# Optimization experiments

Measured on AMD Instinct MI355X. Metric: run time of the kernel, lower is better.

Reference implementation:

```python
import jax, jax.numpy as jnp
import numpy as np

B, N, M = 4, 1024, 3072          # batch, latent (query) len, prefix context len
D, H, DH, L, F = 512, 8, 64, 6, 2048  # dim, heads, dim_head, depth, ff hidden
SCALE = DH ** -0.5


def _ln(x, g, b):
    m = jnp.mean(x, axis=-1, keepdims=True)
    v = jnp.mean(jnp.square(x - m), axis=-1, keepdims=True)
    return (x - m) * jax.lax.rsqrt(v + 1e-5) * g + b


def _heads(t):  # [b, n, h*d] -> [b, h, n, d]
    b, n, _ = t.shape
    return t.reshape(b, n, H, DH).transpose(0, 2, 1, 3)


def _attend(q, k, v):
    # q:[b,h,i,d], k/v:[b,h,j,d]; causal mask triu(j-i+1) as in source
    i, j = q.shape[2], k.shape[2]
    sim = jnp.einsum('bhid,bhjd->bhij', q * SCALE, k)
    mask = jnp.triu(jnp.ones((i, j), dtype=bool), j - i + 1)
    sim = jnp.where(mask, -jnp.finfo(sim.dtype).max, sim)
    attn = jax.nn.softmax(sim, axis=-1)
    out = jnp.einsum('bhij,bhjd->bhid', attn, v)
    return out.transpose(0, 2, 1, 3).reshape(q.shape[0], i, H * DH)


def _ff(x, g, b, w1, w2):
    return jax.nn.gelu(_ln(x, g, b) @ w1, approximate=False) @ w2


def setup_inputs() -> dict:
    key = jax.random.key(0)
    ks = jax.random.split(key, 12)
    rn = lambda k, shape: jax.random.normal(k, shape, dtype=jnp.float32) * 0.02
    return {
        'x': jax.random.normal(ks[0], (B, N, D), jnp.float32),
        'context': jax.random.normal(ks[1], (B, M, D), jnp.float32),
        'pa_norm_g': jnp.ones((D,), jnp.float32), 'pa_norm_b': jnp.zeros((D,), jnp.float32),
        'pa_cnorm_g': jnp.ones((D,), jnp.float32), 'pa_cnorm_b': jnp.zeros((D,), jnp.float32),
        'pa_wq': rn(ks[2], (D, H * DH)), 'pa_wkv': rn(ks[3], (D, 2 * H * DH)),
        'pa_wo': rn(ks[4], (H * DH, D)), 'pa_wo_b': jnp.zeros((D,), jnp.float32),
        'pf_ln_g': jnp.ones((D,), jnp.float32), 'pf_ln_b': jnp.zeros((D,), jnp.float32),
        'pf_w1': rn(ks[5], (D, F)), 'pf_w2': rn(ks[6], (F, D)),
        'sa_ln_g': jnp.ones((L, D), jnp.float32), 'sa_ln_b': jnp.zeros((L, D), jnp.float32),
        'sa_wqkv': rn(ks[7], (L, D, 3 * H * DH)), 'sa_wo': rn(ks[8], (L, H * DH, D)),
        'sf_ln_g': jnp.ones((L, D), jnp.float32), 'sf_ln_b': jnp.zeros((L, D), jnp.float32),
        'sf_w1': rn(ks[9], (L, D, F)), 'sf_w2': rn(ks[10], (L, F, D)),
    }


def reference(x, context, pa_norm_g, pa_norm_b, pa_cnorm_g, pa_cnorm_b,
              pa_wq, pa_wkv, pa_wo, pa_wo_b, pf_ln_g, pf_ln_b, pf_w1, pf_w2,
              sa_ln_g, sa_ln_b, sa_wqkv, sa_wo, sf_ln_g, sf_ln_b, sf_w1, sf_w2):
    # --- CausalPrefixAttention (eval mode: no dropout, context_mask=None) ---
    xn = _ln(x, pa_norm_g, pa_norm_b)
    cn = _ln(context, pa_cnorm_g, pa_cnorm_b)
    q = _heads(xn @ pa_wq)
    k_in, v_in = jnp.split(xn @ pa_wkv, 2, axis=-1)
    k_c, v_c = jnp.split(cn @ pa_wkv, 2, axis=-1)
    k = _heads(jnp.concatenate([k_c, k_in], axis=1))  # [b,h,M+N,d]
    v = _heads(jnp.concatenate([v_c, v_in], axis=1))
    x = _attend(q, k, v) @ pa_wo + pa_wo_b + x
    x = _ff(x, pf_ln_g, pf_ln_b, pf_w1, pf_w2) + x
    # --- depth x (CausalAttention + FeedForward) ---
    for l in range(L):
        xn = _ln(x, sa_ln_g[l], sa_ln_b[l])
        qq, kk, vv = jnp.split(xn @ sa_wqkv[l], 3, axis=-1)
        x = _attend(_heads(qq), _heads(kk), _heads(vv)) @ sa_wo[l] + x
        x = _ff(x, sf_ln_g[l], sf_ln_b[l], sf_w1[l], sf_w2[l]) + x
    return x
```

## Files before the change

### kernel.cpp

```cpp
#include <hip/hip_runtime.h>
#include <hip/hip_bf16.h>
#include <cstdint>
#include <cstddef>

typedef __bf16 bf16;
typedef __attribute__((ext_vector_type(8))) __bf16 bf16x8;
typedef __attribute__((ext_vector_type(4))) __bf16 bf16x4;
typedef __attribute__((ext_vector_type(4))) float f32x4;

constexpr int B_ = 4, QN = 1024, MCTX = 3072, D_ = 512, H_ = 8, DHE = 64, L_ = 6, FF_ = 2048;
constexpr float SCL2_ = 0.18033688011f;

__device__ __forceinline__ f32x4 mfma16(bf16x8 a, bf16x8 b, f32x4 c) {
  return __builtin_amdgcn_mfma_f32_16x16x32_bf16(a, b, c, 0, 0, 0);
}

__device__ __forceinline__ void gl_lds16(const bf16* g, bf16* l) {
  __builtin_amdgcn_global_load_lds((const __attribute__((address_space(1))) void*)g,
                                   (__attribute__((address_space(3))) void*)l, 16, 0, 0);
}

__device__ __forceinline__ float fexp2(float x) {
  float r;
  asm("v_exp_f32 %0, %1" : "=v"(r) : "v"(x));
  return r;
}

__global__ __launch_bounds__(256) void ln_kernel(const float* __restrict__ x,
                                                 const float* __restrict__ g,
                                                 const float* __restrict__ b,
                                                 bf16* __restrict__ out, int rows) {
  int wid = threadIdx.x >> 6, lane = threadIdx.x & 63;
  int row = blockIdx.x * 4 + wid;
  if (row >= rows) return;
  const float* xr = x + (size_t)row * D_;
  f32x4 a0 = *(const f32x4*)(xr + lane * 8);
  f32x4 a1 = *(const f32x4*)(xr + lane * 8 + 4);
  float s = 0.f;
#pragma unroll
  for (int i = 0; i < 4; i++) { s += a0[i]; s += a1[i]; }
#pragma unroll
  for (int d = 1; d < 64; d <<= 1) s += __shfl_xor(s, d);
  float mean = s * (1.0f / 512.0f);
  float q = 0.f;
#pragma unroll
  for (int i = 0; i < 4; i++) {
    float t0 = a0[i] - mean, t1 = a1[i] - mean;
    q += t0 * t0 + t1 * t1;
  }
#pragma unroll
  for (int d = 1; d < 64; d <<= 1) q += __shfl_xor(q, d);
  float rstd = rsqrtf(q * (1.0f / 512.0f) + 1e-5f);
  f32x4 g0 = *(const f32x4*)(g + lane * 8);
  f32x4 g1 = *(const f32x4*)(g + lane * 8 + 4);
  f32x4 b0 = *(const f32x4*)(b + lane * 8);
  f32x4 b1 = *(const f32x4*)(b + lane * 8 + 4);
  bf16x8 o;
#pragma unroll
  for (int i = 0; i < 4; i++) {
    o[i] = (bf16)((a0[i] - mean) * rstd * g0[i] + b0[i]);
    o[i + 4] = (bf16)((a1[i] - mean) * rstd * g1[i] + b1[i]);
  }
  *(bf16x8*)(out + (size_t)row * D_ + lane * 8) = o;
}

struct WDesc { const float* src; bf16* dst; int K; int N; int tstart; };
struct WPack { WDesc d[30]; int n; };

__global__ __launch_bounds__(256) void wtrans_all(WPack p) {
  __shared__ float tile[64][65];
  const int bid = blockIdx.x;
  int mi = 0;
  for (int i = 1; i < p.n; i++)
    if (p.d[i].tstart <= bid) mi = i;
  const float* src = p.d[mi].src;
  bf16* dst = p.d[mi].dst;
  const int K = p.d[mi].K, N = p.d[mi].N;
  const int lt = bid - p.d[mi].tstart;
  const int ntx = N >> 6;
  const int n0 = (lt % ntx) * 64, k0 = (lt / ntx) * 64;
  const int tx = threadIdx.x, ty = threadIdx.y;
#pragma unroll
  for (int pp = 0; pp < 16; pp++)
    tile[pp * 4 + ty][tx] = src[(size_t)(k0 + pp * 4 + ty) * N + n0 + tx];
  __syncthreads();
#pragma unroll
  for (int pp = 0; pp < 16; pp++)
    dst[(size_t)(n0 + pp * 4 + ty) * K + k0 + tx] = (bf16)tile[tx][pp * 4 + ty];
}

template <int EPI>
__global__ __launch_bounds__(256) void gemm128(const bf16* __restrict__ A,
                                               const bf16* __restrict__ BT,
                                               void* __restrict__ C0,
                                               void* __restrict__ C1,
                                               void* __restrict__ C2,
                                               const float* __restrict__ resid,
                                               const float* __restrict__ bias,
                                               int M, int N, int K, int vstr) {
  __shared__ bf16 smA[2][128 * 64];
  __shared__ bf16 smB[2][128 * 64];
  const int tid = threadIdx.x, wid = tid >> 6, lane = tid & 63;
  const int lr = lane & 15, lg = lane >> 4;
  const int tm = blockIdx.y * 128, tn = blockIdx.x * 128;
  const int wr = (wid >> 1) * 64, wc = (wid & 1) * 64;

  const int l3 = lane >> 3;
  const int kslot = ((lane & 7) ^ l3) * 8;
  const bf16* gA[4];
  const bf16* gB[4];
#pragma unroll
  for (int j = 0; j < 4; j++) {
    gA[j] = A + (size_t)(tm + wid * 32 + j * 8 + l3) * K + kslot;
    gB[j] = BT + (size_t)(tn + wid * 32 + j * 8 + l3) * K + kslot;
  }

  f32x4 acc[4][4] = {};
  const int nt = K >> 6;

  auto stage = [&](int bi, int kt) {
#pragma unroll
    for (int j = 0; j < 4; j++) {
      gl_lds16(gA[j] + kt, &smA[bi][(wid * 32 + j * 8) * 64]);
      gl_lds16(gB[j] + kt, &smB[bi][(wid * 32 + j * 8) * 64]);
    }
  };

  stage(0, 0);
  int buf = 0;
  for (int t = 0; t < nt; ++t) {
    asm volatile("s_waitcnt vmcnt(0)" ::: "memory");
    __builtin_amdgcn_s_barrier();
    __builtin_amdgcn_sched_barrier(0);
    if (t + 1 < nt) stage(buf ^ 1, (t + 1) * 64);

    bf16x8 af[4][2], bfr[4][2];
#pragma unroll
    for (int i = 0; i < 4; i++) {
      const int row = wr + i * 16 + lr;
#pragma unroll
      for (int kk = 0; kk < 2; kk++)
        af[i][kk] = *(const bf16x8*)(&smA[buf][row * 64 + (((kk * 4 + lg) ^ (row & 7)) * 8)]);
    }
#pragma unroll
    for (int j = 0; j < 4; j++) {
      const int row = wc + j * 16 + lr;
#pragma unroll
      for (int kk = 0; kk < 2; kk++)
        bfr[j][kk] = *(const bf16x8*)(&smB[buf][row * 64 + (((kk * 4 + lg) ^ (row & 7)) * 8)]);
    }
#pragma unroll
    for (int kk = 0; kk < 2; kk++)
#pragma unroll
      for (int i = 0; i < 4; i++)
#pragma unroll
        for (int j = 0; j < 4; j++)
          acc[i][j] = mfma16(af[i][kk], bfr[j][kk], acc[i][j]);
    buf ^= 1;
  }

  const bool row_major_dst =
      (EPI == 1) || (EPI == 3 && tn < 1024) || (EPI == 4 && tn < 1024) || (EPI == 5 && tn < 512);
  if (row_major_dst) {
    bf16* dst;
    int dstr, rbase, coff;
    if (EPI == 1) { dst = (bf16*)C0; dstr = N; rbase = tm; coff = tn; }
    else if (EPI == 3) {
      if (tn < 512) { dst = (bf16*)C0; dstr = 512; rbase = tm; coff = tn; }
      else { dst = (bf16*)C1; dstr = 1024; rbase = (tm >> 10) * 4096 + (tm & 1023) + 3072; coff = tn - 512; }
    } else if (EPI == 4) { dst = (bf16*)C0; dstr = 1536; rbase = tm; coff = tn; }
    else { dst = (bf16*)C1; dstr = 1024; rbase = (tm / 3072) * 4096 + (tm % 3072); coff = tn; }

    __syncthreads();
    bf16* lb = &smA[0][0];
#pragma unroll
    for (int i = 0; i < 4; i++) {
#pragma unroll
      for (int r = 0; r < 4; r++) {
        const int row = wr + i * 16 + lg * 4 + r;
#pragma unroll
        for (int j = 0; j < 4; j++) {
          const int col = wc + j * 16 + lr;
          float v = acc[i][j][r];
          if (EPI == 1) {
            float u = v * (0.7978845608f + 0.0356774081f * v * v);
            float e = fexp2(fminf(2.885390082f * u, 80.0f));
            v = v * e / (1.0f + e);
          }
          lb[row * 128 + (col ^ ((row & 7) << 3))] = (bf16)v;
        }
      }
    }
    __syncthreads();
#pragma unroll
    for (int p = 0; p < 8; p++) {
      const int row = p * 16 + (tid >> 4);
      const int cb = (tid & 15) * 8;
      bf16x8 v = *(const bf16x8*)&lb[row * 128 + (cb ^ ((row & 7) << 3))];
      *(bf16x8*)&dst[(size_t)(rbase + row) * dstr + coff + cb] = v;
    }
  } else {
#pragma unroll
    for (int i = 0; i < 4; i++) {
      const int row = tm + wr + i * 16 + lg * 4;
#pragma unroll
      for (int j = 0; j < 4; j++) {
        const int col = tn + wc + j * 16 + lr;
        bf16x4 pk = {(bf16)acc[i][j][0], (bf16)acc[i][j][1],
                     (bf16)acc[i][j][2], (bf16)acc[i][j][3]};
        if (EPI == 3) {
          const int cc = col - 1024, hh = cc >> 6, dh = cc & 63;
          const int bb = row >> 10, s = (row & 1023) + 3072;
          *(bf16x4*)&((bf16*)C2)[((size_t)(bb * 8 + hh) * 64 + dh) * vstr + s] = pk;
        } else if (EPI == 4) {
          const int cc = col - 1024, hh = cc >> 6, dh = cc & 63;
          const int bb = row >> 10, s = row & 1023;
          *(bf16x4*)&((bf16*)C2)[((size_t)(bb * 8 + hh) * 64 + dh) * vstr + s] = pk;
        } else {
          const int bq = row / 3072, s = row - bq * 3072;
          const int cc = col - 512, hh = cc >> 6, dh = cc & 63;
          *(bf16x4*)&((bf16*)C2)[((size_t)(bq * 8 + hh) * 64 + dh) * vstr + s] = pk;
        }
      }
    }
  }
}

__global__ __launch_bounds__(256) void gemm64_res(const bf16* __restrict__ A,
                                                  const bf16* __restrict__ BT,
                                                  float* __restrict__ Cout,
                                                  const float* __restrict__ resid,
                                                  const float* __restrict__ bias,
                                                  int M, int N, int K) {
  __shared__ bf16 smA[3][64 * 64];
  __shared__ bf16 smB[3][64 * 64];
  const int tid = threadIdx.x, wid = tid >> 6, lane = tid & 63;
  const int lr = lane & 15, lg = lane >> 4;
  const int tm = blockIdx.y * 64, tn = blockIdx.x * 64;
  const int wr = (wid >> 1) * 32, wc = (wid & 1) * 32;

  const int l3 = lane >> 3;
  const int kslot = ((lane & 7) ^ l3) * 8;
  const int row0 = 2 * wid * 8 + l3;
  const bf16* gA0 = A + (size_t)(tm + row0) * K + kslot;
  const bf16* gA1 = A + (size_t)(tm + row0 + 8) * K + kslot;
  const bf16* gB0 = BT + (size_t)(tn + row0) * K + kslot;
  const bf16* gB1 = BT + (size_t)(tn + row0 + 8) * K + kslot;

  f32x4 acc[2][2] = {};
  const int nt = K >> 6;

  auto stage = [&](int bi, int kt) {
    gl_lds16(gA0 + kt, &smA[bi][(2 * wid) * 512]);
    gl_lds16(gA1 + kt, &smA[bi][(2 * wid + 1) * 512]);
    gl_lds16(gB0 + kt, &smB[bi][(2 * wid) * 512]);
    gl_lds16(gB1 + kt, &smB[bi][(2 * wid + 1) * 512]);
  };

  stage(0, 0);
  if (nt > 1) stage(1, 64);

  for (int t = 0; t < nt; ++t) {
    const int bi = t % 3;
    if (t + 1 < nt) {
      asm volatile("s_waitcnt vmcnt(4)" ::: "memory");
    } else {
      asm volatile("s_waitcnt vmcnt(0)" ::: "memory");
    }
    __builtin_amdgcn_s_barrier();
    __builtin_amdgcn_sched_barrier(0);
    if (t + 2 < nt) stage((t + 2) % 3, (t + 2) * 64);

    bf16x8 af[2][2], bfr[2][2];
#pragma unroll
    for (int i = 0; i < 2; i++) {
      const int row = wr + i * 16 + lr;
#pragma unroll
      for (int kk = 0; kk < 2; kk++)
        af[i][kk] = *(const bf16x8*)(&smA[bi][row * 64 + (((kk * 4 + lg) ^ (row & 7)) * 8)]);
    }
#pragma unroll
    for (int j = 0; j < 2; j++) {
      const int row = wc + j * 16 + lr;
#pragma unroll
      for (int kk = 0; kk < 2; kk++)
        bfr[j][kk] = *(const bf16x8*)(&smB[bi][row * 64 + (((kk * 4 + lg) ^ (row & 7)) * 8)]);
    }
#pragma unroll
    for (int kk = 0; kk < 2; kk++)
#pragma unroll
      for (int i = 0; i < 2; i++)
#pragma unroll
        for (int j = 0; j < 2; j++)
          acc[i][j] = mfma16(af[i][kk], bfr[j][kk], acc[i][j]);
  }

  __syncthreads();
  float* lbuf = (float*)&smA[0][0];
#pragma unroll
  for (int i = 0; i < 2; i++) {
#pragma unroll
    for (int r = 0; r < 4; r++) {
      const int row = wr + i * 16 + lg * 4 + r;
#pragma unroll
      for (int j = 0; j < 2; j++)
        lbuf[row * 68 + wc + j * 16 + lr] = acc[i][j][r];
    }
  }
  __syncthreads();
#pragma unroll
  for (int p = 0; p < 4; p++) {
    const int row = p * 16 + (tid >> 4);
    const int col = (tid & 15) * 4;
    f32x4 v = *(const f32x4*)&lbuf[row * 68 + col];
    const size_t gidx = (size_t)(tm + row) * N + tn + col;
    f32x4 rs = *(const f32x4*)&resid[gidx];
    if (bias) {
      f32x4 bs = *(const f32x4*)&bias[tn + col];
#pragma unroll
      for (int e = 0; e < 4; e++) v[e] += bs[e];
    }
#pragma unroll
    for (int e = 0; e < 4; e++) v[e] += rs[e];
    *(f32x4*)&Cout[gidx] = v;
  }
}

template <int NSPLIT>
__global__ __launch_bounds__(512) void attn_kernel(const bf16* __restrict__ q, int qstride,
                                                   const bf16* __restrict__ k, int kstride,
                                                   const bf16* __restrict__ vt,
                                                   bf16* __restrict__ out,
                                                   bf16* __restrict__ po,
                                                   float* __restrict__ pm,
                                                   float* __restrict__ pl,
                                                   int Skv, int Moff, int spllen) {
  __shared__ bf16 kls[2][4096];
  __shared__ bf16 vls[2][4096];
  __shared__ bf16 pls[8][1024];

  const int tid = threadIdx.x, wid = tid >> 6, lane = tid & 63;
  const int lr = lane & 15, lg = lane >> 4, lg4 = lg * 4;
  const int b = blockIdx.z, h = blockIdx.y;
  const int qblk = blockIdx.x / NSPLIT;
  const int split = blockIdx.x % NSPLIT;
  const int q0b = qblk * 128;
  const int q0w = q0b + wid * 16;
  const int kv_lo = split * spllen;

  int jhi_blk = Moff + q0b + 127;
  if (jhi_blk > Skv - 1) jhi_blk = Skv - 1;
  int hi = kv_lo + spllen;
  if (hi > jhi_blk + 1) hi = jhi_blk + 1;
  const int ntl = (hi > kv_lo) ? ((hi - kv_lo + 63) >> 6) : 0;

  if (NSPLIT > 1 && ntl == 0) {
    size_t rb = ((size_t)split * B_ * H_ + (size_t)b * H_ + h) * QN + q0w;
    const int row = lane >> 2;
    bf16x8 z = {};
#pragma unroll
    for (int half = 0; half < 2; half++)
      *(bf16x8*)&po[(rb + row) * 64 + (lane & 3) * 16 + half * 8] = z;
    if (lg == 0) { pm[rb + lr] = -3e38f; pl[rb + lr] = 0.f; }
    return;
  }

  const int sel = ((tid >> 6) & 1) * 32 + ((tid >> 4) & 3) * 8;
  const int srow0 = (tid >> 7) * 16 + (tid & 15);
  const bf16* kbase = k + (size_t)b * Skv * kstride + h * DHE + sel;
  const bf16* vbase = vt + (size_t)((b * H_ + h) * DHE) * Skv + sel;

  const bf16* qp = q + (size_t)(b * QN + q0w + lr) * qstride + h * DHE;
  bf16x8 qa0 = *(const bf16x8*)(qp + lg * 8);
  bf16x8 qa1 = *(const bf16x8*)(qp + 32 + lg * 8);
#pragma unroll
  for (int i = 0; i < 8; i++) {
    qa0[i] = (bf16)((float)qa0[i] * SCL2_);
    qa1[i] = (bf16)((float)qa1[i] * SCL2_);
  }
  bf16x8 vones;
#pragma unroll
  for (int i = 0; i < 8; i++) vones[i] = (bf16)1.0f;

  f32x4 o[4] = {};
  f32x4 o4 = {};

  auto stage = [&](int bi, int j0) {
    gl_lds16(kbase + (size_t)(j0 + srow0) * kstride, &kls[bi][tid * 8]);
    gl_lds16(vbase + (size_t)srow0 * Skv + j0, &vls[bi][tid * 8]);
  };

  stage(0, kv_lo);
  __syncthreads();
  int buf = 0;
  bf16* pw = &pls[wid][0];

  for (int t = 0; t < ntl; ++t) {
    const int j0 = kv_lo + t * 64;
    if (t + 1 < ntl) stage(buf ^ 1, j0 + 64);
    const bf16* kbp = &kls[buf][0];
    const bf16* vbp = &vls[buf][0];

    f32x4 sv[4];
    __builtin_amdgcn_s_setprio(1);
#pragma unroll
    for (int kg = 0; kg < 4; kg++) {
      bf16x8 k0 = *(const bf16x8*)(kbp + (kg * 128 + lane) * 8);
      bf16x8 k1 = *(const bf16x8*)(kbp + (kg * 128 + 64 + lane) * 8);
      f32x4 z = {0.f, 0.f, 0.f, 0.f};
      z = mfma16(k0, qa0, z);
      z = mfma16(k1, qa1, z);
      sv[kg] = z;
    }
    __builtin_amdgcn_s_setprio(0);
    const bool full = (j0 + 63 <= Moff + q0w);
    if (!full) {
      const int limq = Moff + q0w + lr;
#pragma unroll
      for (int kg = 0; kg < 4; kg++)
#pragma unroll
        for (int r = 0; r < 4; r++)
          if (j0 + kg * 16 + lg4 + r > limq) sv[kg][r] = -3e38f;
    }
#pragma unroll
    for (int kg = 0; kg < 4; kg++) {
      float p0 = fexp2(sv[kg][0]);
      float p1 = fexp2(sv[kg][1]);
      float p2 = fexp2(sv[kg][2]);
      float p3 = fexp2(sv[kg][3]);
      bf16x4 pk = {(bf16)p0, (bf16)p1, (bf16)p2, (bf16)p3};
      const int k8 = kg * 2 + (lg >> 1);
      *(bf16x4*)(pw + ((k8 >> 2) * 64 + (k8 & 3) * 16 + lr) * 8 + (lg & 1) * 4) = pk;
    }
    bf16x8 pa0 = *(const bf16x8*)(pw + lane * 8);
    bf16x8 pa1 = *(const bf16x8*)(pw + (64 + lane) * 8);
    __builtin_amdgcn_s_setprio(1);
#pragma unroll
    for (int f = 0; f < 4; f++) {
      bf16x8 v0 = *(const bf16x8*)(vbp + (f * 128 + lane) * 8);
      bf16x8 v1 = *(const bf16x8*)(vbp + (f * 128 + 64 + lane) * 8);
      o[f] = mfma16(pa0, v0, o[f]);
      o[f] = mfma16(pa1, v1, o[f]);
    }
    o4 = mfma16(pa0, vones, o4);
    o4 = mfma16(pa1, vones, o4);
    __builtin_amdgcn_s_setprio(0);
    __syncthreads();
    buf ^= 1;
  }

  if (NSPLIT == 1) {
    float li[4];
#pragma unroll
    for (int r = 0; r < 4; r++) li[r] = 1.0f / o4[r];
#pragma unroll
    for (int f = 0; f < 4; f++)
#pragma unroll
      for (int r = 0; r < 4; r++) {
        const int row = lg4 + r, col = f * 16 + lr;
        pw[row * 64 + (col ^ ((row & 7) << 3))] = (bf16)(o[f][r] * li[r]);
      }
    const int row = lane >> 2;
#pragma unroll
    for (int half = 0; half < 2; half++) {
      const int cb = (lane & 3) * 16 + half * 8;
      bf16x8 v = *(const bf16x8*)&pw[row * 64 + (cb ^ ((row & 7) << 3))];
      *(bf16x8*)&out[(size_t)(b * QN + q0w + row) * D_ + h * DHE + cb] = v;
    }
  } else {
    size_t rb = ((size_t)split * B_ * H_ + (size_t)b * H_ + h) * QN + q0w;
#pragma unroll
    for (int f = 0; f < 4; f++)
#pragma unroll
      for (int r = 0; r < 4; r++) {
        const int row = lg4 + r, col = f * 16 + lr;
        pw[row * 64 + (col ^ ((row & 7) << 3))] = (bf16)o[f][r];
      }
    const int row = lane >> 2;
#pragma unroll
    for (int half = 0; half < 2; half++) {
      const int cb = (lane & 3) * 16 + half * 8;
      bf16x8 v = *(const bf16x8*)&pw[row * 64 + (cb ^ ((row & 7) << 3))];
      *(bf16x8*)&po[(rb + row) * 64 + cb] = v;
    }
    if (lr == 0) {
#pragma unroll
      for (int r = 0; r < 4; r++) {
        pm[rb + lg4 + r] = 0.f;
        pl[rb + lg4 + r] = o4[r];
      }
    }
  }
}

template <int NSPLIT>
__global__ __launch_bounds__(256) void attn_combine(const bf16* __restrict__ po,
                                                    const float* __restrict__ pm,
                                                    const float* __restrict__ pl,
                                                    bf16* __restrict__ out) {
  constexpr int TOT = B_ * H_ * QN;
  const int wid = threadIdx.x >> 6, lane = threadIdx.x & 63;
  const int row = blockIdx.x * 4 + wid;
  float mv[NSPLIT], lv[NSPLIT];
  float mstar = -3e38f;
#pragma unroll
  for (int s = 0; s < NSPLIT; s++) {
    mv[s] = pm[s * TOT + row];
    lv[s] = pl[s * TOT + row];
    mstar = fmaxf(mstar, mv[s]);
  }
  float lstar = 0.f, acc = 0.f;
#pragma unroll
  for (int s = 0; s < NSPLIT; s++) {
    float w = fexp2(mv[s] - mstar);
    lstar += lv[s] * w;
    acc += (float)po[((size_t)s * TOT + row) * 64 + lane] * w;
  }
  const int b = row >> 13, hq = row & 8191, h = hq >> 10, qq = hq & 1023;
  out[((size_t)b * QN + qq) * D_ + h * DHE + lane] = (bf16)(acc / lstar);
}

extern "C" void kernel_launch(void* const* d_in, const int* in_sizes, int n_in,
                              void* d_out, int out_size, void* d_ws, size_t ws_size,
                              hipStream_t stream) {
  const float* x       = (const float*)d_in[0];
  const float* ctx     = (const float*)d_in[1];
  const float* pa_ng   = (const float*)d_in[2];
  const float* pa_nb   = (const float*)d_in[3];
  const float* pa_cg   = (const float*)d_in[4];
  const float* pa_cb   = (const float*)d_in[5];
  const float* pa_wq   = (const float*)d_in[6];
  const float* pa_wkv  = (const float*)d_in[7];
  const float* pa_wo   = (const float*)d_in[8];
  const float* pa_wob  = (const float*)d_in[9];
  const float* pf_g    = (const float*)d_in[10];
  const float* pf_b    = (const float*)d_in[11];
  const float* pf_w1   = (const float*)d_in[12];
  const float* pf_w2   = (const float*)d_in[13];
  const float* sa_g    = (const float*)d_in[14];
  const float* sa_b    = (const float*)d_in[15];
  const float* sa_wqkv = (const float*)d_in[16];
  const float* sa_wo   = (const float*)d_in[17];
  const float* sf_g    = (const float*)d_in[18];
  const float* sf_b    = (const float*)d_in[19];
  const float* sf_w1   = (const float*)d_in[20];
  const float* sf_w2   = (const float*)d_in[21];
  float* xo = (float*)d_out;

  char* ws = (char*)d_ws;
  size_t off = 0;
  auto alloc = [&](size_t bytes) -> char* {
    char* p = ws + off;
    off += (bytes + 255) & ~(size_t)255;
    return p;
  };

  bf16* wqT    = (bf16*)alloc((size_t)512 * 512 * 2);
  bf16* wkvT   = (bf16*)alloc((size_t)1024 * 512 * 2);
  bf16* woT    = (bf16*)alloc((size_t)512 * 512 * 2);
  bf16* w1T    = (bf16*)alloc((size_t)2048 * 512 * 2);
  bf16* w2T    = (bf16*)alloc((size_t)512 * 2048 * 2);
  bf16* saqkvT = (bf16*)alloc((size_t)L_ * 1536 * 512 * 2);
  bf16* sawoT  = (bf16*)alloc((size_t)L_ * 512 * 512 * 2);
  bf16* sfw1T  = (bf16*)alloc((size_t)L_ * 2048 * 512 * 2);
  bf16* sfw2T  = (bf16*)alloc((size_t)L_ * 512 * 2048 * 2);
  bf16* xn    = (bf16*)alloc((size_t)4096 * 512 * 2);
  bf16* reg1  = (bf16*)alloc((size_t)12288 * 512 * 2);
  bf16* qb    = (bf16*)alloc((size_t)4096 * 512 * 2);
  bf16* reg2  = (bf16*)alloc((size_t)B_ * 4096 * 1024 * 2);
  bf16* vtb   = (bf16*)alloc((size_t)B_ * H_ * 64 * 4096 * 2);
  bf16* attnb = (bf16*)alloc((size_t)4096 * 512 * 2);
  constexpr int NSPL = 4;
  constexpr int TOTR = B_ * H_ * QN;
  bf16* po = (bf16*)alloc((size_t)NSPL * TOTR * 64 * 2);
  float* pmb = (float*)alloc((size_t)NSPL * TOTR * 4);
  float* plb = (float*)alloc((size_t)NSPL * TOTR * 4);
  const bool use_split = (off <= ws_size);
  bf16* cn = reg1;
  bf16* qkvb = reg1;
  bf16* kvb = reg2;
  bf16* ffh = reg2;
  (void)in_sizes; (void)n_in; (void)out_size;

  WPack wp;
  int nt_acc = 0, wi = 0;
  auto addw = [&](const float* s, bf16* d, int K, int N) {
    wp.d[wi].src = s; wp.d[wi].dst = d; wp.d[wi].K = K; wp.d[wi].N = N;
    wp.d[wi].tstart = nt_acc;
    nt_acc += (N / 64) * (K / 64);
    wi++;
  };
  addw(pa_wq, wqT, 512, 512);
  addw(pa_wkv, wkvT, 512, 1024);
  addw(pa_wo, woT, 512, 512);
  addw(pf_w1, w1T, 512, 2048);
  addw(pf_w2, w2T, 2048, 512);
  for (int l = 0; l < L_; l++) {
    addw(sa_wqkv + (size_t)l * 512 * 1536, saqkvT + (size_t)l * 1536 * 512, 512, 1536);
    addw(sa_wo + (size_t)l * 512 * 512, sawoT + (size_t)l * 512 * 512, 512, 512);
    addw(sf_w1 + (size_t)l * 512 * 2048, sfw1T + (size_t)l * 2048 * 512, 512, 2048);
    addw(sf_w2 + (size_t)l * 2048 * 512, sfw2T + (size_t)l * 512 * 2048, 2048, 512);
  }
  wp.n = wi;
  wtrans_all<<<nt_acc, dim3(64, 4, 1), 0, stream>>>(wp);

  ln_kernel<<<1024, 256, 0, stream>>>(x, pa_ng, pa_nb, xn, 4096);
  ln_kernel<<<3072, 256, 0, stream>>>(ctx, pa_cg, pa_cb, cn, 12288);
  hipLaunchKernelGGL(HIP_KERNEL_NAME(gemm128<5>), dim3(1024 / 128, 12288 / 128), dim3(256), 0,
                     stream, cn, wkvT, nullptr, kvb, vtb, nullptr, nullptr, 12288, 1024, 512, 4096);
  hipLaunchKernelGGL(HIP_KERNEL_NAME(gemm128<3>), dim3(1536 / 128, 4096 / 128), dim3(256), 0,
                     stream, xn, wqT, qb, kvb, vtb, nullptr, nullptr, 4096, 1536, 512, 4096);
  if (use_split) {
    hipLaunchKernelGGL(HIP_KERNEL_NAME(attn_kernel<NSPL>), dim3((QN / 128) * NSPL, H_, B_), dim3(512), 0,
                       stream, qb, 512, kvb, 1024, vtb, attnb, po, pmb, plb, 4096, MCTX, 1024);
    hipLaunchKernelGGL(HIP_KERNEL_NAME(attn_combine<NSPL>), dim3(TOTR / 4), dim3(256), 0,
                       stream, po, pmb, plb, attnb);
  } else {
    hipLaunchKernelGGL(HIP_KERNEL_NAME(attn_kernel<1>), dim3(QN / 128, H_, B_), dim3(512), 0,
                       stream, qb, 512, kvb, 1024, vtb, attnb, po, pmb, plb, 4096, MCTX, 4096);
  }
  gemm64_res<<<dim3(512 / 64, 4096 / 64), 256, 0, stream>>>(attnb, woT, xo, x, pa_wob, 4096, 512, 512);
  ln_kernel<<<1024, 256, 0, stream>>>(xo, pf_g, pf_b, xn, 4096);
  hipLaunchKernelGGL(HIP_KERNEL_NAME(gemm128<1>), dim3(2048 / 128, 4096 / 128), dim3(256), 0,
                     stream, xn, w1T, ffh, nullptr, nullptr, nullptr, nullptr, 4096, 2048, 512, 0);
  gemm64_res<<<dim3(512 / 64, 4096 / 64), 256, 0, stream>>>(ffh, w2T, xo, xo, nullptr, 4096, 512, 2048);

  for (int l = 0; l < L_; l++) {
    ln_kernel<<<1024, 256, 0, stream>>>(xo, sa_g + l * 512, sa_b + l * 512, xn, 4096);
    hipLaunchKernelGGL(HIP_KERNEL_NAME(gemm128<4>), dim3(1536 / 128, 4096 / 128), dim3(256), 0,
                       stream, xn, saqkvT + (size_t)l * 1536 * 512, qkvb, nullptr, vtb,
                       nullptr, nullptr, 4096, 1536, 512, 1024);
    if (use_split) {
      hipLaunchKernelGGL(HIP_KERNEL_NAME(attn_kernel<2>), dim3((QN / 128) * 2, H_, B_), dim3(512), 0,
                         stream, qkvb, 1536, qkvb + 512, 1536, vtb, attnb, po, pmb, plb, 1024, 0, 512);
      hipLaunchKernelGGL(HIP_KERNEL_NAME(attn_combine<2>), dim3(TOTR / 4), dim3(256), 0,
                         stream, po, pmb, plb, attnb);
    } else {
      hipLaunchKernelGGL(HIP_KERNEL_NAME(attn_kernel<1>), dim3(QN / 128, H_, B_), dim3(512), 0,
                         stream, qkvb, 1536, qkvb + 512, 1536, vtb, attnb, po, pmb, plb, 1024, 0, 1024);
    }
    gemm64_res<<<dim3(512 / 64, 4096 / 64), 256, 0, stream>>>(attnb, sawoT + (size_t)l * 512 * 512,
                                                              xo, xo, nullptr, 4096, 512, 512);
    ln_kernel<<<1024, 256, 0, stream>>>(xo, sf_g + l * 512, sf_b + l * 512, xn, 4096);
    hipLaunchKernelGGL(HIP_KERNEL_NAME(gemm128<1>), dim3(2048 / 128, 4096 / 128), dim3(256), 0,
                       stream, xn, sfw1T + (size_t)l * 2048 * 512, ffh, nullptr, nullptr,
                       nullptr, nullptr, 4096, 2048, 512, 0);
    gemm64_res<<<dim3(512 / 64, 4096 / 64), 256, 0, stream>>>(ffh, sfw2T + (size_t)l * 512 * 2048,
                                                              xo, xo, nullptr, 4096, 512, 2048);
  }
}
```

Baseline: 771.2 us.

## Use triple-buffered BK=32 pipeline in gemm128 and intra-block split-K residual GEMM

gemm128 moves from a double-buffered K=64 tile to a triple-buffered K=32 tile with a two-stage-ahead prefetch and partial vmcnt waits, so loads overlap more with MFMA work. The residual GEMM is replaced by gemm64k2: 512 threads split each 128-wide K chunk between two wave groups, and the partial sums are reduced through LDS before the residual/bias epilogue. The goal is more latency hiding and more waves per output tile for the narrow N=512 GEMMs. The cost is more barriers per K step, an extra LDS reduction pass, and higher LDS use per block.

```diff
diff --git a/kernel.cpp b/kernel.cpp
--- a/kernel.cpp
+++ b/kernel.cpp
@@ -98,65 +98,61 @@
                                                const float* __restrict__ resid,
                                                const float* __restrict__ bias,
                                                int M, int N, int K, int vstr) {
-  __shared__ bf16 smA[2][128 * 64];
-  __shared__ bf16 smB[2][128 * 64];
+  __shared__ bf16 sm[6 * 4096];
+  bf16* sA = sm;
+  bf16* sB = sm + 3 * 4096;
   const int tid = threadIdx.x, wid = tid >> 6, lane = tid & 63;
   const int lr = lane & 15, lg = lane >> 4;
   const int tm = blockIdx.y * 128, tn = blockIdx.x * 128;
   const int wr = (wid >> 1) * 64, wc = (wid & 1) * 64;
 
-  const int l3 = lane >> 3;
-  const int kslot = ((lane & 7) ^ l3) * 8;
-  const bf16* gA[4];
-  const bf16* gB[4];
-#pragma unroll
-  for (int j = 0; j < 4; j++) {
-    gA[j] = A + (size_t)(tm + wid * 32 + j * 8 + l3) * K + kslot;
-    gB[j] = BT + (size_t)(tn + wid * 32 + j * 8 + l3) * K + kslot;
-  }
+  const int r0 = tid >> 2, ls0 = tid & 3;
+  const int gs0 = ls0 ^ (r0 & 3);
+  const bf16* gA0 = A + (size_t)(tm + r0) * K + gs0 * 8;
+  const bf16* gB0 = BT + (size_t)(tn + r0) * K + gs0 * 8;
+  const bf16* gA1 = gA0 + (size_t)64 * K;
+  const bf16* gB1 = gB0 + (size_t)64 * K;
 
   f32x4 acc[4][4] = {};
-  const int nt = K >> 6;
+  const int nt = K >> 5;
 
   auto stage = [&](int bi, int kt) {
-#pragma unroll
-    for (int j = 0; j < 4; j++) {
-      gl_lds16(gA[j] + kt, &smA[bi][(wid * 32 + j * 8) * 64]);
-      gl_lds16(gB[j] + kt, &smB[bi][(wid * 32 + j * 8) * 64]);
-    }
+    gl_lds16(gA0 + kt, sA + bi * 4096 + tid * 8);
+    gl_lds16(gA1 + kt, sA + bi * 4096 + (tid + 256) * 8);
+    gl_lds16(gB0 + kt, sB + bi * 4096 + tid * 8);
+    gl_lds16(gB1 + kt, sB + bi * 4096 + (tid + 256) * 8);
   };
 
   stage(0, 0);
-  int buf = 0;
+  stage(1, 32);
+
   for (int t = 0; t < nt; ++t) {
-    asm volatile("s_waitcnt vmcnt(0)" ::: "memory");
+    const int bi = t % 3;
+    if (t + 1 < nt) {
+      asm volatile("s_waitcnt vmcnt(4)" ::: "memory");
+    } else {
+      asm volatile("s_waitcnt vmcnt(0)" ::: "memory");
+    }
     __builtin_amdgcn_s_barrier();
     __builtin_amdgcn_sched_barrier(0);
-    if (t + 1 < nt) stage(buf ^ 1, (t + 1) * 64);
-
-    bf16x8 af[4][2], bfr[4][2];
+    if (t + 2 < nt) stage((t + 2) % 3, (t + 2) * 32);
+
+    bf16x8 af[4], bfr[4];
 #pragma unroll
     for (int i = 0; i < 4; i++) {
       const int row = wr + i * 16 + lr;
-#pragma unroll
-      for (int kk = 0; kk < 2; kk++)
-        af[i][kk] = *(const bf16x8*)(&smA[buf][row * 64 + (((kk * 4 + lg) ^ (row & 7)) * 8)]);
+      af[i] = *(const bf16x8*)&sA[bi * 4096 + row * 32 + ((lg ^ (row & 3)) * 8)];
     }
 #pragma unroll
     for (int j = 0; j < 4; j++) {
       const int row = wc + j * 16 + lr;
-#pragma unroll
-      for (int kk = 0; kk < 2; kk++)
-        bfr[j][kk] = *(const bf16x8*)(&smB[buf][row * 64 + (((kk * 4 + lg) ^ (row & 7)) * 8)]);
-    }
-#pragma unroll
-    for (int kk = 0; kk < 2; kk++)
-#pragma unroll
-      for (int i = 0; i < 4; i++)
-#pragma unroll
-        for (int j = 0; j < 4; j++)
-          acc[i][j] = mfma16(af[i][kk], bfr[j][kk], acc[i][j]);
-    buf ^= 1;
+      bfr[j] = *(const bf16x8*)&sB[bi * 4096 + row * 32 + ((lg ^ (row & 3)) * 8)];
+    }
+#pragma unroll
+    for (int i = 0; i < 4; i++)
+#pragma unroll
+      for (int j = 0; j < 4; j++)
+        acc[i][j] = mfma16(af[i], bfr[j], acc[i][j]);
   }
 
   const bool row_major_dst =
@@ -172,7 +168,7 @@
     else { dst = (bf16*)C1; dstr = 1024; rbase = (tm / 3072) * 4096 + (tm % 3072); coff = tn; }
 
     __syncthreads();
-    bf16* lb = &smA[0][0];
+    bf16* lb = sm;
 #pragma unroll
     for (int i = 0; i < 4; i++) {
 #pragma unroll
@@ -226,65 +222,62 @@
   }
 }
 
-__global__ __launch_bounds__(256) void gemm64_res(const bf16* __restrict__ A,
-                                                  const bf16* __restrict__ BT,
-                                                  float* __restrict__ Cout,
-                                                  const float* __restrict__ resid,
-                                                  const float* __restrict__ bias,
-                                                  int M, int N, int K) {
-  __shared__ bf16 smA[3][64 * 64];
-  __shared__ bf16 smB[3][64 * 64];
+__global__ __launch_bounds__(512) void gemm64k2(const bf16* __restrict__ A,
+                                                const bf16* __restrict__ BT,
+                                                float* __restrict__ Cout,
+                                                const float* __restrict__ resid,
+                                                const float* __restrict__ bias,
+                                                int M, int N, int K) {
+  __shared__ bf16 sm[2][2][64 * 128];
   const int tid = threadIdx.x, wid = tid >> 6, lane = tid & 63;
   const int lr = lane & 15, lg = lane >> 4;
   const int tm = blockIdx.y * 64, tn = blockIdx.x * 64;
-  const int wr = (wid >> 1) * 32, wc = (wid & 1) * 32;
-
-  const int l3 = lane >> 3;
-  const int kslot = ((lane & 7) ^ l3) * 8;
-  const int row0 = 2 * wid * 8 + l3;
-  const bf16* gA0 = A + (size_t)(tm + row0) * K + kslot;
-  const bf16* gA1 = A + (size_t)(tm + row0 + 8) * K + kslot;
-  const bf16* gB0 = BT + (size_t)(tn + row0) * K + kslot;
-  const bf16* gB1 = BT + (size_t)(tn + row0 + 8) * K + kslot;
+  const int ws = wid >> 2;
+  const int wq = wid & 3;
+  const int wr = (wq >> 1) * 32, wc = (wq & 1) * 32;
+
+  const int r0 = tid >> 4, u0 = tid & 7, h0 = (tid >> 3) & 1;
+  const int g0 = h0 * 8 + (u0 ^ (r0 & 7));
+  const bf16* gA0 = A + (size_t)(tm + r0) * K + g0 * 8;
+  const bf16* gB0 = BT + (size_t)(tn + r0) * K + g0 * 8;
+  const bf16* gA1 = gA0 + (size_t)32 * K;
+  const bf16* gB1 = gB0 + (size_t)32 * K;
+
+  auto stage = [&](int bi, int kt) {
+    gl_lds16(gA0 + kt, &sm[bi][0][tid * 8]);
+    gl_lds16(gA1 + kt, &sm[bi][0][(tid + 512) * 8]);
+    gl_lds16(gB0 + kt, &sm[bi][1][tid * 8]);
+    gl_lds16(gB1 + kt, &sm[bi][1][(tid + 512) * 8]);
+  };
 
   f32x4 acc[2][2] = {};
-  const int nt = K >> 6;
-
-  auto stage = [&](int bi, int kt) {
-    gl_lds16(gA0 + kt, &smA[bi][(2 * wid) * 512]);
-    gl_lds16(gA1 + kt, &smA[bi][(2 * wid + 1) * 512]);
-    gl_lds16(gB0 + kt, &smB[bi][(2 * wid) * 512]);
-    gl_lds16(gB1 + kt, &smB[bi][(2 * wid + 1) * 512]);
-  };
-
+  const int nt = K >> 7;
   stage(0, 0);
-  if (nt > 1) stage(1, 64);
-
+  int buf = 0;
   for (int t = 0; t < nt; ++t) {
-    const int bi = t % 3;
-    if (t + 1 < nt) {
-      asm volatile("s_waitcnt vmcnt(4)" ::: "memory");
-    } else {
-      asm volatile("s_waitcnt vmcnt(0)" ::: "memory");
-    }
+    asm volatile("s_waitcnt vmcnt(0)" ::: "memory");
     __builtin_amdgcn_s_barrier();
     __builtin_amdgcn_sched_barrier(0);
-    if (t + 2 < nt) stage((t + 2) % 3, (t + 2) * 64);
+    if (t + 1 < nt) stage(buf ^ 1, (t + 1) * 128);
 
     bf16x8 af[2][2], bfr[2][2];
 #pragma unroll
     for (int i = 0; i < 2; i++) {
       const int row = wr + i * 16 + lr;
 #pragma unroll
-      for (int kk = 0; kk < 2; kk++)
-        af[i][kk] = *(const bf16x8*)(&smA[bi][row * 64 + (((kk * 4 + lg) ^ (row & 7)) * 8)]);
+      for (int kk = 0; kk < 2; kk++) {
+        const int slot = ws * 8 + ((kk * 4 + lg) ^ (row & 7));
+        af[i][kk] = *(const bf16x8*)&sm[buf][0][row * 128 + slot * 8];
+      }
     }
 #pragma unroll
     for (int j = 0; j < 2; j++) {
       const int row = wc + j * 16 + lr;
 #pragma unroll
-      for (int kk = 0; kk < 2; kk++)
-        bfr[j][kk] = *(const bf16x8*)(&smB[bi][row * 64 + (((kk * 4 + lg) ^ (row & 7)) * 8)]);
+      for (int kk = 0; kk < 2; kk++) {
+        const int slot = ws * 8 + ((kk * 4 + lg) ^ (row & 7));
+        bfr[j][kk] = *(const bf16x8*)&sm[buf][1][row * 128 + slot * 8];
+      }
     }
 #pragma unroll
     for (int kk = 0; kk < 2; kk++)
@@ -293,24 +286,38 @@
 #pragma unroll
         for (int j = 0; j < 2; j++)
           acc[i][j] = mfma16(af[i][kk], bfr[j][kk], acc[i][j]);
+    buf ^= 1;
   }
 
   __syncthreads();
-  float* lbuf = (float*)&smA[0][0];
-#pragma unroll
-  for (int i = 0; i < 2; i++) {
-#pragma unroll
-    for (int r = 0; r < 4; r++) {
-      const int row = wr + i * 16 + lg * 4 + r;
-#pragma unroll
-      for (int j = 0; j < 2; j++)
-        lbuf[row * 68 + wc + j * 16 + lr] = acc[i][j][r];
-    }
+  float* lbuf = (float*)&sm[0][0][0];
+  if (ws == 0) {
+#pragma unroll
+    for (int i = 0; i < 2; i++)
+#pragma unroll
+      for (int r = 0; r < 4; r++) {
+        const int row = wr + i * 16 + lg * 4 + r;
+#pragma unroll
+        for (int j = 0; j < 2; j++)
+          lbuf[row * 68 + wc + j * 16 + lr] = acc[i][j][r];
+      }
   }
   __syncthreads();
-#pragma unroll
-  for (int p = 0; p < 4; p++) {
-    const int row = p * 16 + (tid >> 4);
+  if (ws == 1) {
+#pragma unroll
+    for (int i = 0; i < 2; i++)
+#pragma unroll
+      for (int r = 0; r < 4; r++) {
+        const int row = wr + i * 16 + lg * 4 + r;
+#pragma unroll
+        for (int j = 0; j < 2; j++)
+          lbuf[row * 68 + wc + j * 16 + lr] += acc[i][j][r];
+      }
+  }
+  __syncthreads();
+#pragma unroll
+  for (int p = 0; p < 2; p++) {
+    const int row = p * 32 + (tid >> 4);
     const int col = (tid & 15) * 4;
     f32x4 v = *(const f32x4*)&lbuf[row * 68 + col];
     const size_t gidx = (size_t)(tm + row) * N + tn + col;
@@ -619,11 +626,11 @@
     hipLaunchKernelGGL(HIP_KERNEL_NAME(attn_kernel<1>), dim3(QN / 128, H_, B_), dim3(512), 0,
                        stream, qb, 512, kvb, 1024, vtb, attnb, po, pmb, plb, 4096, MCTX, 4096);
   }
-  gemm64_res<<<dim3(512 / 64, 4096 / 64), 256, 0, stream>>>(attnb, woT, xo, x, pa_wob, 4096, 512, 512);
+  gemm64k2<<<dim3(512 / 64, 4096 / 64), 512, 0, stream>>>(attnb, woT, xo, x, pa_wob, 4096, 512, 512);
   ln_kernel<<<1024, 256, 0, stream>>>(xo, pf_g, pf_b, xn, 4096);
   hipLaunchKernelGGL(HIP_KERNEL_NAME(gemm128<1>), dim3(2048 / 128, 4096 / 128), dim3(256), 0,
                      stream, xn, w1T, ffh, nullptr, nullptr, nullptr, nullptr, 4096, 2048, 512, 0);
-  gemm64_res<<<dim3(512 / 64, 4096 / 64), 256, 0, stream>>>(ffh, w2T, xo, xo, nullptr, 4096, 512, 2048);
+  gemm64k2<<<dim3(512 / 64, 4096 / 64), 512, 0, stream>>>(ffh, w2T, xo, xo, nullptr, 4096, 512, 2048);
 
   for (int l = 0; l < L_; l++) {
     ln_kernel<<<1024, 256, 0, stream>>>(xo, sa_g + l * 512, sa_b + l * 512, xn, 4096);
@@ -639,13 +646,13 @@
       hipLaunchKernelGGL(HIP_KERNEL_NAME(attn_kernel<1>), dim3(QN / 128, H_, B_), dim3(512), 0,
                          stream, qkvb, 1536, qkvb + 512, 1536, vtb, attnb, po, pmb, plb, 1024, 0, 1024);
     }
-    gemm64_res<<<dim3(512 / 64, 4096 / 64), 256, 0, stream>>>(attnb, sawoT + (size_t)l * 512 * 512,
-                                                              xo, xo, nullptr, 4096, 512, 512);
+    gemm64k2<<<dim3(512 / 64, 4096 / 64), 512, 0, stream>>>(attnb, sawoT + (size_t)l * 512 * 512,
+                                                            xo, xo, nullptr, 4096, 512, 512);
     ln_kernel<<<1024, 256, 0, stream>>>(xo, sf_g + l * 512, sf_b + l * 512, xn, 4096);
     hipLaunchKernelGGL(HIP_KERNEL_NAME(gemm128<1>), dim3(2048 / 128, 4096 / 128), dim3(256), 0,
                        stream, xn, sfw1T + (size_t)l * 2048 * 512, ffh, nullptr, nullptr,
                        nullptr, nullptr, 4096, 2048, 512, 0);
-    gemm64_res<<<dim3(512 / 64, 4096 / 64), 256, 0, stream>>>(ffh, sfw2T + (size_t)l * 512 * 2048,
-                                                              xo, xo, nullptr, 4096, 512, 2048);
-  }
-}
+    gemm64k2<<<dim3(512 / 64, 4096 / 64), 512, 0, stream>>>(ffh, sfw2T + (size_t)l * 512 * 2048,
+                                                            xo, xo, nullptr, 4096, 512, 2048);
+  }
+}
```

Measured after the change: 752.7 us. 2.4% less time.
